# Kernel tuning notes

Hardware: AMD Instinct MI355X
Metric: run time of the kernel (lower is better)

Reference implementation:

```python
import jax, jax.numpy as jnp
import numpy as np


def setup_inputs() -> dict:
    key = jax.random.key(0)
    ks = jax.random.split(key, 5)
    B, T, D, U = 32, 2048, 512, 512
    scale = 1.0 / np.sqrt(D)
    return {
        "full": jax.random.normal(ks[0], (B, T, D), jnp.float32),
        "last": jax.random.normal(ks[1], (B, D), jnp.float32),
        "W1": jax.random.normal(ks[2], (D, U), jnp.float32) * scale,
        "b1": jnp.zeros((U,), jnp.float32),
        "W2": jax.random.normal(ks[3], (D, U), jnp.float32) * scale,
        "b2": jnp.zeros((U,), jnp.float32),
        "V": jax.random.normal(ks[4], (U, 1), jnp.float32) * (1.0 / np.sqrt(U)),
        "bV": jnp.zeros((1,), jnp.float32),
    }


def reference(full, last, W1, b1, W2, b2, V, bV):
    # full: [B,T,D], last: [B,D]
    h1 = jnp.einsum("btd,du->btu", full, W1) + b1          # [B,T,U]
    h2 = last @ W2 + b2                                      # [B,U]
    score = jnp.tanh(h1 + h2[:, None, :]) @ V + bV           # [B,T,1]
    attn = jax.nn.softmax(score, axis=1)                     # [B,T,1]
    context = jnp.sum(attn * full, axis=1)                   # [B,D]
    return context
```

## Files before the change

kernel.cpp:

```cpp
#include <hip/hip_runtime.h>
#include <math.h>


#define BB 32
#define TT 2048
#define DD 512
#define UU 512

typedef short bf16x8 __attribute__((ext_vector_type(8)));
typedef float f32x4  __attribute__((ext_vector_type(4)));

static __device__ __forceinline__ short f2bf(float f) {
    unsigned x = __float_as_uint(f);
    return (short)((x + 0x7fffu + ((x >> 16) & 1u)) >> 16);
}

static __device__ __forceinline__ float fast_tanh(float x) {
    float e = __expf(2.f * x);
    return 1.f - 2.f * __builtin_amdgcn_rcpf(e + 1.f);
}

__global__ __launch_bounds__(256) void prep_kernel(const float* __restrict__ W1,
                                                   short* __restrict__ W1T,
                                                   const float* __restrict__ last,
                                                   const float* __restrict__ W2,
                                                   const float* __restrict__ b1,
                                                   const float* __restrict__ b2,
                                                   float* __restrict__ h2) {
    __shared__ float tile[32][33];
    __shared__ float ls[DD];
    __shared__ float part[256];
    const int bid = blockIdx.x;
    const int tid = threadIdx.x;
    if (bid < 256) {
        const int tr = (bid >> 4) << 5;
        const int tc = (bid & 15) << 5;
#pragma unroll
        for (int p = 0; p < 4; ++p) {
            const int r = p * 8 + (tid >> 5), c = tid & 31;
            tile[r][c] = W1[(size_t)(tr + r) * UU + tc + c];
        }
        __syncthreads();
#pragma unroll
        for (int p = 0; p < 4; ++p) {
            const int r = p * 8 + (tid >> 5), c = tid & 31;
            W1T[(size_t)(tc + r) * DD + tr + c] = f2bf(tile[c][r]);
        }
    } else {
        const int b2i = bid - 256;
        const int b  = b2i >> 2;
        const int u0 = (b2i & 3) << 7;
        for (int i = tid; i < DD; i += 256) ls[i] = last[b * DD + i];
        __syncthreads();
        const int uu = tid & 127;
        const int dh = tid >> 7;
        float acc = 0.f;
#pragma unroll 8
        for (int d = dh * 256; d < dh * 256 + 256; ++d)
            acc += ls[d] * W2[d * UU + u0 + uu];
        part[tid] = acc;
        __syncthreads();
        if (tid < 128) {
            const int u = u0 + tid;
            h2[b * UU + u] = part[tid] + part[tid + 128] + b1[u] + b2[u];
        }
    }
}

__global__ __launch_bounds__(512) void score_kernel(const float* __restrict__ full,
                                                    const short* __restrict__ W1T,
                                                    const float* __restrict__ h2,
                                                    const float* __restrict__ V,
                                                    float* __restrict__ ctx,
                                                    float* __restrict__ m_arr,
                                                    float* __restrict__ l_arr) {
    __shared__ __align__(16) float a32[128 * 64];
    __shared__ __align__(16) short blds[512 * 64];
    __shared__ float red64[8][64];
    __shared__ float esc[128];
    __shared__ float sred[8];
    __shared__ __align__(16) float red4[4][128][4];

    const int bid = blockIdx.x;
    const int b    = bid >> 4;
    const int t0   = (bid & 15) << 7;
    const int tid  = threadIdx.x;
    const int w    = tid >> 6;
    const int lane = tid & 63;
    const int quad = lane >> 4;
    const int col  = lane & 15;
    const int wm   = w >> 2;
    const int wn   = w & 3;

    f32x4 acc[4][8];
#pragma unroll
    for (int i = 0; i < 4; ++i)
#pragma unroll
        for (int j = 0; j < 8; ++j) acc[i][j] = (f32x4){0.f, 0.f, 0.f, 0.f};

    const size_t fullbase = (size_t)(b * TT + t0) * DD;

    for (int ko = 0; ko < 8; ++ko) {
        if (ko) __syncthreads();
#pragma unroll
        for (int i = 0; i < 4; ++i) {
            const int sb = w * 256 + i * 64;
            const int s  = sb + lane;
            const int r  = s >> 4;
            const int cc = (s & 15) ^ (r & 15);
            const float* g = &full[fullbase + (size_t)r * DD + ko * 64 + cc * 4];
            __builtin_amdgcn_global_load_lds(
                (const __attribute__((address_space(1))) void*)g,
                (__attribute__((address_space(3))) void*)&a32[sb * 4], 16, 0, 0);
        }
#pragma unroll
        for (int i = 0; i < 8; ++i) {
            const int sb = w * 512 + i * 64;
            const int s  = sb + lane;
            const int u  = s >> 3;
            const int kc = (s & 7) ^ (u & 7);
            const short* g = &W1T[(size_t)u * DD + ko * 64 + kc * 8];
            __builtin_amdgcn_global_load_lds(
                (const __attribute__((address_space(1))) void*)g,
                (__attribute__((address_space(3))) void*)&blds[sb * 8], 16, 0, 0);
        }
        __syncthreads();

#pragma unroll
        for (int ki = 0; ki < 2; ++ki) {
            bf16x8 af[4];
#pragma unroll
            for (int mt = 0; mt < 4; ++mt) {
                const int r   = wm * 64 + mt * 16 + col;
                const int cc0 = ki * 8 + quad * 2;
                const f32x4 lo = *(const f32x4*)&a32[(r * 16 + (cc0 ^ (r & 15))) * 4];
                const f32x4 hi = *(const f32x4*)&a32[(r * 16 + ((cc0 + 1) ^ (r & 15))) * 4];
                af[mt] = (bf16x8){f2bf(lo.x), f2bf(lo.y), f2bf(lo.z), f2bf(lo.w),
                                  f2bf(hi.x), f2bf(hi.y), f2bf(hi.z), f2bf(hi.w)};
            }
#pragma unroll
            for (int nt = 0; nt < 8; ++nt) {
                const int u  = wn * 128 + nt * 16 + col;
                const int kc = ki * 4 + quad;
                const bf16x8 bf = *(const bf16x8*)&blds[(u * 8 + (kc ^ (u & 7))) * 8];
#pragma unroll
                for (int mt = 0; mt < 4; ++mt)
                    acc[mt][nt] = __builtin_amdgcn_mfma_f32_16x16x32_bf16(af[mt], bf, acc[mt][nt], 0, 0, 0);
            }
        }
    }

    float srow[16];
#pragma unroll
    for (int i = 0; i < 16; ++i) srow[i] = 0.f;
#pragma unroll
    for (int nt = 0; nt < 8; ++nt) {
        const int u = wn * 128 + nt * 16 + col;
        const float hv = h2[b * UU + u];
        const float vv = V[u];
#pragma unroll
        for (int mt = 0; mt < 4; ++mt)
#pragma unroll
            for (int r = 0; r < 4; ++r)
                srow[mt * 4 + r] += fast_tanh(acc[mt][nt][r] + hv) * vv;
    }
#pragma unroll
    for (int off = 1; off < 16; off <<= 1) {
#pragma unroll
        for (int i = 0; i < 16; ++i) srow[i] += __shfl_xor(srow[i], off, 64);
    }
    if (col == 0) {
#pragma unroll
        for (int mt = 0; mt < 4; ++mt)
#pragma unroll
            for (int r = 0; r < 4; ++r)
                red64[w][mt * 16 + quad * 4 + r] = srow[mt * 4 + r];
    }
    __syncthreads();

    float sv = 0.f;
    if (tid < 128) {
        const int wmX = tid >> 6, rr = tid & 63;
        sv = red64[wmX * 4 + 0][rr] + red64[wmX * 4 + 1][rr] +
             red64[wmX * 4 + 2][rr] + red64[wmX * 4 + 3][rr];
        float mv = sv;
#pragma unroll
        for (int off = 1; off < 64; off <<= 1) mv = fmaxf(mv, __shfl_xor(mv, off, 64));
        if (lane == 0) sred[w] = mv;
    }
    __syncthreads();
    const float M = fmaxf(sred[0], sred[1]);
    if (tid < 128) {
        float e = __expf(sv - M);
        esc[tid] = e;
#pragma unroll
        for (int off = 1; off < 64; off <<= 1) e += __shfl_xor(e, off, 64);
        if (lane == 0) sred[4 + w] = e;
    }
    __syncthreads();
    if (tid == 0) { m_arr[bid] = M; l_arr[bid] = sred[4] + sred[5]; }

    const int c  = tid & 127;
    const int tp = tid >> 7;
    float ax = 0.f, ay = 0.f, az = 0.f, aw = 0.f;
#pragma unroll 4
    for (int i = 0; i < 32; ++i) {
        const int t = i * 4 + tp;
        const float4 v = *(const float4*)&full[fullbase + (size_t)t * DD + c * 4];
        const float e = esc[t];
        ax += e * v.x; ay += e * v.y; az += e * v.z; aw += e * v.w;
    }
    *(float4*)&red4[tp][c][0] = make_float4(ax, ay, az, aw);
    __syncthreads();
    if (tp == 0) {
        const float4 p0 = *(const float4*)&red4[0][c][0];
        const float4 p1 = *(const float4*)&red4[1][c][0];
        const float4 p2 = *(const float4*)&red4[2][c][0];
        const float4 p3 = *(const float4*)&red4[3][c][0];
        float4 s = make_float4(p0.x + p1.x + p2.x + p3.x,
                               p0.y + p1.y + p2.y + p3.y,
                               p0.z + p1.z + p2.z + p3.z,
                               p0.w + p1.w + p2.w + p3.w);
        *(float4*)&ctx[(size_t)bid * DD + c * 4] = s;
    }
}

__global__ __launch_bounds__(256) void combine_kernel(const float* __restrict__ ctx,
                                                      const float* __restrict__ m_arr,
                                                      const float* __restrict__ l_arr,
                                                      float* __restrict__ out) {
    const int b = blockIdx.x;
    const int tid = threadIdx.x;
    __shared__ float wgt[16];
    __shared__ float linv;
    if (tid == 0) {
        float M = -1e30f;
#pragma unroll
        for (int i = 0; i < 16; ++i) M = fmaxf(M, m_arr[b * 16 + i]);
        float l = 0.f;
#pragma unroll
        for (int i = 0; i < 16; ++i) {
            wgt[i] = __expf(m_arr[b * 16 + i] - M);
            l += wgt[i] * l_arr[b * 16 + i];
        }
        linv = 1.f / l;
    }
    __syncthreads();
    float s0 = 0.f, s1 = 0.f;
#pragma unroll
    for (int i = 0; i < 16; ++i) {
        const float wi = wgt[i];
        const float* cp = &ctx[(size_t)(b * 16 + i) * DD + tid * 2];
        s0 += wi * cp[0];
        s1 += wi * cp[1];
    }
    out[b * DD + tid * 2]     = s0 * linv;
    out[b * DD + tid * 2 + 1] = s1 * linv;
}

extern "C" void kernel_launch(void* const* d_in, const int* in_sizes, int n_in,
                              void* d_out, int out_size, void* d_ws, size_t ws_size,
                              hipStream_t stream) {
    const float* full = (const float*)d_in[0];
    const float* last = (const float*)d_in[1];
    const float* W1   = (const float*)d_in[2];
    const float* b1   = (const float*)d_in[3];
    const float* W2   = (const float*)d_in[4];
    const float* b2   = (const float*)d_in[5];
    const float* V    = (const float*)d_in[6];

    float* out   = (float*)d_out;
    float* h2    = (float*)d_ws;
    float* m_arr = h2 + (size_t)BB * UU;
    float* l_arr = m_arr + 512;
    float* ctx   = l_arr + 512;
    short* W1T   = (short*)(ctx + (size_t)BB * 16 * DD);

    prep_kernel<<<384, 256, 0, stream>>>(W1, W1T, last, W2, b1, b2, h2);
    score_kernel<<<BB * 16, 512, 0, stream>>>(full, W1T, h2, V, ctx, m_arr, l_arr);
    combine_kernel<<<BB, 256, 0, stream>>>(ctx, m_arr, l_arr, out);
}
```

Measured before the change: 270.4 us.

## Double-buffer LDS tiles with smaller K-step to overlap loads and MFMA

Splits the K loop into 16 steps of 32 instead of 8 steps of 64 and double-buffers the A (fp32 activations) and B (bf16 W1T) tiles in LDS. The next tile is prefetched via global_load_lds while MFMAs run on the current buffer, leaving one barrier per step. The swizzle patterns are adapted to the narrower tile width. LDS use stays about the same, but there are twice as many barriers and each stage has fewer MFMAs to hide load latency behind.

```diff
diff --git a/kernel.cpp b/kernel.cpp
--- a/kernel.cpp
+++ b/kernel.cpp
@@ -6,6 +6,8 @@
 #define TT 2048
 #define DD 512
 #define UU 512
+#define BKK 32
+#define KSTEPS 16
 
 typedef short bf16x8 __attribute__((ext_vector_type(8)));
 typedef float f32x4  __attribute__((ext_vector_type(4)));
@@ -74,8 +76,8 @@
                                                     float* __restrict__ ctx,
                                                     float* __restrict__ m_arr,
                                                     float* __restrict__ l_arr) {
-    __shared__ __align__(16) float a32[128 * 64];
-    __shared__ __align__(16) short blds[512 * 64];
+    __shared__ __align__(16) float a32[2][128 * BKK];
+    __shared__ __align__(16) short blds[2][512 * BKK];
     __shared__ float red64[8][64];
     __shared__ float esc[128];
     __shared__ float sred[8];
@@ -100,55 +102,60 @@
 
     const size_t fullbase = (size_t)(b * TT + t0) * DD;
 
-    for (int ko = 0; ko < 8; ++ko) {
-        if (ko) __syncthreads();
-#pragma unroll
-        for (int i = 0; i < 4; ++i) {
-            const int sb = w * 256 + i * 64;
-            const int s  = sb + lane;
-            const int r  = s >> 4;
-            const int cc = (s & 15) ^ (r & 15);
-            const float* g = &full[fullbase + (size_t)r * DD + ko * 64 + cc * 4];
-            __builtin_amdgcn_global_load_lds(
-                (const __attribute__((address_space(1))) void*)g,
-                (__attribute__((address_space(3))) void*)&a32[sb * 4], 16, 0, 0);
-        }
-#pragma unroll
-        for (int i = 0; i < 8; ++i) {
-            const int sb = w * 512 + i * 64;
-            const int s  = sb + lane;
-            const int u  = s >> 3;
-            const int kc = (s & 7) ^ (u & 7);
-            const short* g = &W1T[(size_t)u * DD + ko * 64 + kc * 8];
-            __builtin_amdgcn_global_load_lds(
-                (const __attribute__((address_space(1))) void*)g,
-                (__attribute__((address_space(3))) void*)&blds[sb * 8], 16, 0, 0);
-        }
-        __syncthreads();
-
-#pragma unroll
-        for (int ki = 0; ki < 2; ++ki) {
-            bf16x8 af[4];
-#pragma unroll
-            for (int mt = 0; mt < 4; ++mt) {
-                const int r   = wm * 64 + mt * 16 + col;
-                const int cc0 = ki * 8 + quad * 2;
-                const f32x4 lo = *(const f32x4*)&a32[(r * 16 + (cc0 ^ (r & 15))) * 4];
-                const f32x4 hi = *(const f32x4*)&a32[(r * 16 + ((cc0 + 1) ^ (r & 15))) * 4];
-                af[mt] = (bf16x8){f2bf(lo.x), f2bf(lo.y), f2bf(lo.z), f2bf(lo.w),
-                                  f2bf(hi.x), f2bf(hi.y), f2bf(hi.z), f2bf(hi.w)};
-            }
-#pragma unroll
-            for (int nt = 0; nt < 8; ++nt) {
-                const int u  = wn * 128 + nt * 16 + col;
-                const int kc = ki * 4 + quad;
-                const bf16x8 bf = *(const bf16x8*)&blds[(u * 8 + (kc ^ (u & 7))) * 8];
-#pragma unroll
-                for (int mt = 0; mt < 4; ++mt)
-                    acc[mt][nt] = __builtin_amdgcn_mfma_f32_16x16x32_bf16(af[mt], bf, acc[mt][nt], 0, 0, 0);
-            }
-        }
-    }
+#define STAGE(bufidx, koidx) do {                                                     \
+        _Pragma("unroll")                                                             \
+        for (int i = 0; i < 2; ++i) {                                                 \
+            const int sb = w * 128 + i * 64;                                          \
+            const int s  = sb + lane;                                                 \
+            const int r  = s >> 3;                                                    \
+            const int cc = (s & 7) ^ (r & 7);                                         \
+            const float* g = &full[fullbase + (size_t)r * DD + (koidx) * BKK + cc * 4]; \
+            __builtin_amdgcn_global_load_lds(                                         \
+                (const __attribute__((address_space(1))) void*)g,                     \
+                (__attribute__((address_space(3))) void*)&a32[bufidx][sb * 4], 16, 0, 0); \
+        }                                                                             \
+        _Pragma("unroll")                                                             \
+        for (int i = 0; i < 4; ++i) {                                                 \
+            const int sb = w * 256 + i * 64;                                          \
+            const int s  = sb + lane;                                                 \
+            const int u  = s >> 2;                                                    \
+            const int kc = (s & 3) ^ ((u >> 1) & 3);                                  \
+            const short* g = &W1T[(size_t)u * DD + (koidx) * BKK + kc * 8];           \
+            __builtin_amdgcn_global_load_lds(                                         \
+                (const __attribute__((address_space(1))) void*)g,                     \
+                (__attribute__((address_space(3))) void*)&blds[bufidx][sb * 8], 16, 0, 0); \
+        }                                                                             \
+    } while (0)
+
+    STAGE(0, 0);
+    __syncthreads();
+
+    int cur = 0;
+    for (int ko = 0; ko < KSTEPS; ++ko) {
+        if (ko < KSTEPS - 1) STAGE(cur ^ 1, ko + 1);
+
+        bf16x8 af[4];
+#pragma unroll
+        for (int mt = 0; mt < 4; ++mt) {
+            const int r  = wm * 64 + mt * 16 + col;
+            const int c0 = quad * 2;
+            const f32x4 lo = *(const f32x4*)&a32[cur][(r * 8 + (c0 ^ (r & 7))) * 4];
+            const f32x4 hi = *(const f32x4*)&a32[cur][(r * 8 + ((c0 + 1) ^ (r & 7))) * 4];
+            af[mt] = (bf16x8){f2bf(lo.x), f2bf(lo.y), f2bf(lo.z), f2bf(lo.w),
+                              f2bf(hi.x), f2bf(hi.y), f2bf(hi.z), f2bf(hi.w)};
+        }
+#pragma unroll
+        for (int nt = 0; nt < 8; ++nt) {
+            const int u = wn * 128 + nt * 16 + col;
+            const bf16x8 bf = *(const bf16x8*)&blds[cur][(u * 4 + (quad ^ ((u >> 1) & 3))) * 8];
+#pragma unroll
+            for (int mt = 0; mt < 4; ++mt)
+                acc[mt][nt] = __builtin_amdgcn_mfma_f32_16x16x32_bf16(af[mt], bf, acc[mt][nt], 0, 0, 0);
+        }
+        __syncthreads();
+        cur ^= 1;
+    }
+#undef STAGE
 
     float srow[16];
 #pragma unroll
```

After: 264.8 us. 1.02x faster.
